# Performance work log

Hardware: AMD Instinct MI355X
Metric: run time of the kernel (lower is better)

Reference implementation:

```python
import jax, jax.numpy as jnp
import numpy as np

IN_F = 4096
OUT_F = 4096

def setup_inputs() -> dict:
    key = jax.random.key(0)
    k1, k2 = jax.random.split(key)
    x = jax.random.normal(k1, (4, 2048, IN_F), dtype=jnp.float32)
    W = jax.random.normal(k2, (OUT_F, IN_F), dtype=jnp.float32) * (1.0 / np.sqrt(IN_F))
    return {"x": x, "W": W}

def reference(x, W):
    # per-tensor scale = mean |W|, clamped
    scale = jnp.maximum(jnp.mean(jnp.abs(W)), 1e-8)
    # pentanet: 5-level quantization {-2,-1,0,1,2}
    w_quant = jnp.clip(jnp.round(W / scale), -2.0, 2.0)
    # STE: forward uses quantized weights, gradient flows to W
    w_ste = jax.lax.stop_gradient(w_quant * scale - W) + W
    # F.linear: x @ w_ste.T -> [b, s, out]
    return jnp.einsum('bsi,oi->bso', x, w_ste)
```

## Files before the change

kernel.cpp:

```cpp
#include <hip/hip_runtime.h>
#include <cstdint>
#include <cstddef>

#define IN_F 4096
#define OUT_F 4096

typedef __attribute__((ext_vector_type(8))) short bf16x8;
typedef __attribute__((ext_vector_type(4))) float f32x4;

__device__ __forceinline__ ushort f32_bf16_rne(float f) {
    uint32_t u = __builtin_bit_cast(uint32_t, f);
    uint32_t r = (u + 0x7FFFu + ((u >> 16) & 1u)) >> 16;
    return (ushort)r;
}

__device__ __forceinline__ void gload_lds16(const void* g, void* l) {
    __builtin_amdgcn_global_load_lds(
        (const __attribute__((address_space(1))) uint32_t*)g,
        (__attribute__((address_space(3))) uint32_t*)l,
        16, 0, 0);
}

__device__ __forceinline__ void fenced_barrier() {
    asm volatile("" ::: "memory");
    __builtin_amdgcn_sched_barrier(0);
    __builtin_amdgcn_s_barrier();
    __builtin_amdgcn_sched_barrier(0);
    asm volatile("" ::: "memory");
}

__global__ void reduce_abs1(const float* __restrict__ W, float* __restrict__ part) {
    __shared__ float sm[256];
    const int b = blockIdx.x, t = threadIdx.x;
    const float* p = W + (size_t)b * 4096;
    float s = 0.f;
#pragma unroll
    for (int j = 0; j < 16; ++j) s += fabsf(p[t + 256 * j]);
    sm[t] = s;
    __syncthreads();
    for (int w = 128; w > 0; w >>= 1) {
        if (t < w) sm[t] += sm[t + w];
        __syncthreads();
    }
    if (t == 0) part[b] = sm[0];
}

__global__ void reduce_abs2(const float* __restrict__ part, float* __restrict__ scale) {
    __shared__ float sm[256];
    const int t = threadIdx.x;
    float s = 0.f;
#pragma unroll
    for (int j = 0; j < 16; ++j) s += part[t + 256 * j];
    sm[t] = s;
    __syncthreads();
    for (int w = 128; w > 0; w >>= 1) {
        if (t < w) sm[t] += sm[t + w];
        __syncthreads();
    }
    if (t == 0) {
        float m = sm[0] / 16777216.0f;
        *scale = fmaxf(m, 1e-8f);
    }
}

__global__ void quantize_w(const float* __restrict__ W, ushort* __restrict__ wq,
                           const float* __restrict__ scale_p) {
    const int i = blockIdx.x * 256 + threadIdx.x;
    const float s = *scale_p;
    float4 v = ((const float4*)W)[i];
    float q0 = fminf(fmaxf(rintf(v.x / s), -2.f), 2.f);
    float q1 = fminf(fmaxf(rintf(v.y / s), -2.f), 2.f);
    float q2 = fminf(fmaxf(rintf(v.z / s), -2.f), 2.f);
    float q3 = fminf(fmaxf(rintf(v.w / s), -2.f), 2.f);
    ushort4 o;
    o.x = f32_bf16_rne(q0); o.y = f32_bf16_rne(q1);
    o.z = f32_bf16_rne(q2); o.w = f32_bf16_rne(q3);
    ((ushort4*)wq)[i] = o;
}

__global__ void cast_x(const float* __restrict__ X, ushort* __restrict__ xh) {
    const int i = blockIdx.x * 256 + threadIdx.x;
    float4 v = ((const float4*)X)[i];
    ushort4 o;
    o.x = f32_bf16_rne(v.x); o.y = f32_bf16_rne(v.y);
    o.z = f32_bf16_rne(v.z); o.w = f32_bf16_rne(v.w);
    ((ushort4*)xh)[i] = o;
}

#define BK 64
#define HT_BYTES 16384
#define BUF_BYTES 65536

__global__ __launch_bounds__(512, 2) void qgemm256(
        const ushort* __restrict__ Ab, const ushort* __restrict__ Bq,
        float* __restrict__ C, const float* __restrict__ scale_p,
        int M, int N, int K) {
    extern __shared__ __align__(16) char smem[];

    const int t = threadIdx.x;
    const int lane = t & 63;
    const int w = t >> 6;
    const int wr = w >> 2;
    const int wc = w & 3;
    const int bh = wc >> 1;

    const int nwg = gridDim.x;
    int wg = blockIdx.x;
    if ((nwg & 7) == 0) wg = (wg & 7) * (nwg >> 3) + (wg >> 3);
    const int MT = M >> 8;
    const int m0 = (wg % MT) << 8;
    const int n0 = (wg / MT) << 8;

    const int NT = K / BK;
    const int NS = NT * 4;

    int pre[2];
#pragma unroll
    for (int ks = 0; ks < 2; ++ks)
        pre[ks] = (lane & 15) * 128 +
                  (((ks * 64) + ((lane >> 4) * 16)) ^ ((lane & 7) << 4));

    auto do_stage = [&](int s) {
        if (s >= NS) return;
        const int kt = s >> 2, h = s & 3;
        const int k0 = kt * BK;
        char* region;
        const ushort* gsrc;
        if (h < 2) {
            region = smem + (kt & 1) * BUF_BYTES + 32768 + h * HT_BYTES;
            gsrc = Bq + (size_t)(n0 + h * 128) * K + k0;
        } else {
            region = smem + (kt & 1) * BUF_BYTES + (h - 2) * HT_BYTES;
            gsrc = Ab + (size_t)(m0 + (h - 2) * 128) * K + k0;
        }
#pragma unroll
        for (int j = 0; j < 2; ++j) {
            int e = j * 4096 + t * 8;
            int r = e >> 6, c8 = (e >> 3) & 7;
            int srcc = (c8 ^ (r & 7)) * 8;
            gload_lds16(gsrc + (size_t)r * K + srcc, region + e * 2);
        }
    };

    f32x4 acc[8][4];
#pragma unroll
    for (int m = 0; m < 8; ++m)
#pragma unroll
        for (int n = 0; n < 4; ++n) acc[m][n] = (f32x4){0.f, 0.f, 0.f, 0.f};

    do_stage(0); do_stage(1); do_stage(2); do_stage(3);
    asm volatile("s_waitcnt vmcnt(4)");
    do_stage(4); do_stage(5); do_stage(6);
    asm volatile("s_waitcnt vmcnt(6)");
    fenced_barrier();

    for (int kt = 0; kt < NT; ++kt) {
        const char* aB = smem + (kt & 1) * BUF_BYTES + wr * HT_BYTES;
        const char* bB = smem + (kt & 1) * BUF_BYTES + 32768 + bh * HT_BYTES +
                         (wc & 1) * 8192;
        const int sbase = 7 + kt * 4;

        bf16x8 bfr[4][2], a0[4][2], a1[4][2];

#pragma unroll
        for (int n = 0; n < 4; ++n)
#pragma unroll
            for (int ks = 0; ks < 2; ++ks)
                bfr[n][ks] = *(const bf16x8*)(bB + n * 2048 + pre[ks]);
#pragma unroll
        for (int m = 0; m < 4; ++m)
#pragma unroll
            for (int ks = 0; ks < 2; ++ks)
                a0[m][ks] = *(const bf16x8*)(aB + m * 2048 + pre[ks]);
        do_stage(sbase + 0);
        fenced_barrier();
        __builtin_amdgcn_s_setprio(1);
#pragma unroll
        for (int m = 0; m < 4; ++m)
#pragma unroll
            for (int n = 0; n < 2; ++n)
#pragma unroll
                for (int ks = 0; ks < 2; ++ks)
                    acc[m][n] = __builtin_amdgcn_mfma_f32_16x16x32_bf16(
                        a0[m][ks], bfr[n][ks], acc[m][n], 0, 0, 0);
        __builtin_amdgcn_s_setprio(0);
        fenced_barrier();

#pragma unroll
        for (int m = 0; m < 4; ++m)
#pragma unroll
            for (int ks = 0; ks < 2; ++ks)
                a1[m][ks] = *(const bf16x8*)(aB + (m + 4) * 2048 + pre[ks]);
        do_stage(sbase + 1);
        fenced_barrier();
        __builtin_amdgcn_s_setprio(1);
#pragma unroll
        for (int m = 0; m < 4; ++m)
#pragma unroll
            for (int n = 2; n < 4; ++n)
#pragma unroll
                for (int ks = 0; ks < 2; ++ks)
                    acc[m][n] = __builtin_amdgcn_mfma_f32_16x16x32_bf16(
                        a0[m][ks], bfr[n][ks], acc[m][n], 0, 0, 0);
        __builtin_amdgcn_s_setprio(0);
        fenced_barrier();

        do_stage(sbase + 2);
        fenced_barrier();
        __builtin_amdgcn_s_setprio(1);
#pragma unroll
        for (int m = 0; m < 4; ++m)
#pragma unroll
            for (int n = 0; n < 2; ++n)
#pragma unroll
                for (int ks = 0; ks < 2; ++ks)
                    acc[m + 4][n] = __builtin_amdgcn_mfma_f32_16x16x32_bf16(
                        a1[m][ks], bfr[n][ks], acc[m + 4][n], 0, 0, 0);
        __builtin_amdgcn_s_setprio(0);
        fenced_barrier();

        do_stage(sbase + 3);
        fenced_barrier();
        __builtin_amdgcn_s_setprio(1);
#pragma unroll
        for (int m = 0; m < 4; ++m)
#pragma unroll
            for (int n = 2; n < 4; ++n)
#pragma unroll
                for (int ks = 0; ks < 2; ++ks)
                    acc[m + 4][n] = __builtin_amdgcn_mfma_f32_16x16x32_bf16(
                        a1[m][ks], bfr[n][ks], acc[m + 4][n], 0, 0, 0);
        __builtin_amdgcn_s_setprio(0);
        if (kt < NT - 2) {
            asm volatile("s_waitcnt vmcnt(6)");
        } else if (kt == NT - 2) {
            asm volatile("s_waitcnt vmcnt(0)");
        }
        fenced_barrier();
    }

    const float s = *scale_p;
#pragma unroll
    for (int m = 0; m < 8; ++m)
#pragma unroll
        for (int n = 0; n < 4; ++n) {
            const int col = n0 + wc * 64 + n * 16 + (lane & 15);
            const int rbase = m0 + wr * 128 + m * 16 + ((lane >> 4) << 2);
#pragma unroll
            for (int j = 0; j < 4; ++j)
                C[(size_t)(rbase + j) * N + col] = s * acc[m][n][j];
        }
}

template <bool ABF16>
__global__ __launch_bounds__(256) void qgemm(const void* __restrict__ Aptr,
                                             const ushort* __restrict__ Bq,
                                             float* __restrict__ C,
                                             const float* __restrict__ scale_p,
                                             int M, int N, int K) {
    __shared__ __align__(16) ushort sA[128 * 64];
    __shared__ __align__(16) ushort sB[128 * 64];

    const int t = threadIdx.x;
    const int lane = t & 63;
    const int w = t >> 6;
    const int wr = w >> 1, wc = w & 1;

    const int nwg = gridDim.x;
    int wg = blockIdx.x;
    if ((nwg & 7) == 0) wg = (wg & 7) * (nwg >> 3) + (wg >> 3);
    const int MT = M >> 7;
    const int mt = wg % MT;
    const int nt = wg / MT;
    const int m0 = mt * 128, n0 = nt * 128;

    const ushort* Ab = (const ushort*)Aptr;
    const float* Af = (const float*)Aptr;

    f32x4 zero = {0.f, 0.f, 0.f, 0.f};
    f32x4 acc[4][4];
#pragma unroll
    for (int m = 0; m < 4; ++m)
#pragma unroll
        for (int n = 0; n < 4; ++n) acc[m][n] = zero;

    for (int k0 = 0; k0 < K; k0 += 64) {
#pragma unroll
        for (int i = 0; i < 4; ++i) {
            int e = i * 2048 + t * 8;
            int r = e >> 6, c8 = (e >> 3) & 7;
            int srcc = (c8 ^ (r & 7)) * 8;
            gload_lds16(Bq + (size_t)(n0 + r) * K + (k0 + srcc), &sB[e]);
        }
        if constexpr (ABF16) {
#pragma unroll
            for (int i = 0; i < 4; ++i) {
                int e = i * 2048 + t * 8;
                int r = e >> 6, c8 = (e >> 3) & 7;
                int srcc = (c8 ^ (r & 7)) * 8;
                gload_lds16(Ab + (size_t)(m0 + r) * K + (k0 + srcc), &sA[e]);
            }
        } else {
#pragma unroll
            for (int i = 0; i < 4; ++i) {
                int e = i * 2048 + t * 8;
                int r = e >> 6, c = e & 63;
                const float* src = Af + (size_t)(m0 + r) * K + (k0 + c);
                float4 v0 = *(const float4*)src;
                float4 v1 = *(const float4*)(src + 4);
                bf16x8 pk;
                pk[0] = (short)f32_bf16_rne(v0.x); pk[1] = (short)f32_bf16_rne(v0.y);
                pk[2] = (short)f32_bf16_rne(v0.z); pk[3] = (short)f32_bf16_rne(v0.w);
                pk[4] = (short)f32_bf16_rne(v1.x); pk[5] = (short)f32_bf16_rne(v1.y);
                pk[6] = (short)f32_bf16_rne(v1.z); pk[7] = (short)f32_bf16_rne(v1.w);
                int byte = (r * 128 + c * 2) ^ ((r & 7) << 4);
                *(bf16x8*)((char*)sA + byte) = pk;
            }
        }
        __syncthreads();

#pragma unroll
        for (int ks = 0; ks < 2; ++ks) {
            const int kk = ks * 32 + ((lane >> 4) << 3);
            bf16x8 afr[4], bfr[4];
#pragma unroll
            for (int m = 0; m < 4; ++m) {
                int r = wr * 64 + m * 16 + (lane & 15);
                int byte = (r * 128 + kk * 2) ^ ((r & 7) << 4);
                afr[m] = *(const bf16x8*)((const char*)sA + byte);
            }
#pragma unroll
            for (int n = 0; n < 4; ++n) {
                int r = wc * 64 + n * 16 + (lane & 15);
                int byte = (r * 128 + kk * 2) ^ ((r & 7) << 4);
                bfr[n] = *(const bf16x8*)((const char*)sB + byte);
            }
#pragma unroll
            for (int m = 0; m < 4; ++m)
#pragma unroll
                for (int n = 0; n < 4; ++n)
                    acc[m][n] = __builtin_amdgcn_mfma_f32_16x16x32_bf16(
                        afr[m], bfr[n], acc[m][n], 0, 0, 0);
        }
        __syncthreads();
    }

    const float s = *scale_p;
#pragma unroll
    for (int m = 0; m < 4; ++m)
#pragma unroll
        for (int n = 0; n < 4; ++n) {
            const int col = n0 + wc * 64 + n * 16 + (lane & 15);
            const int rbase = m0 + wr * 64 + m * 16 + ((lane >> 4) << 2);
#pragma unroll
            for (int j = 0; j < 4; ++j)
                C[(size_t)(rbase + j) * N + col] = s * acc[m][n][j];
        }
}

__global__ void naive_qgemm(const float* __restrict__ X, const float* __restrict__ W,
                            float* __restrict__ out, const float* __restrict__ scale_p,
                            int M) {
    const int col = blockIdx.x * 256 + threadIdx.x;
    const int row = blockIdx.y;
    const float s = *scale_p;
    const float inv = 1.0f / s;
    const float* xr = X + (size_t)row * IN_F;
    const float* wrow = W + (size_t)col * IN_F;
    float acc = 0.f;
    for (int k = 0; k < IN_F; ++k) {
        float q = fminf(fmaxf(rintf(wrow[k] * inv), -2.f), 2.f);
        acc += xr[k] * q;
    }
    out[(size_t)row * OUT_F + col] = acc * s;
}

extern "C" void kernel_launch(void* const* d_in, const int* in_sizes, int n_in,
                              void* d_out, int out_size, void* d_ws, size_t ws_size,
                              hipStream_t stream) {
    const float* x = (const float*)d_in[0];
    const float* W = (const float*)d_in[1];
    float* out = (float*)d_out;
    const int M = in_sizes[0] / IN_F;
    const int K = IN_F, N = OUT_F;

    char* ws = (char*)d_ws;
    const size_t OFF_PART = 512;
    const size_t OFF_WQ = OFF_PART + 4096 * sizeof(float);
    const size_t WQ_BYTES = (size_t)N * K * sizeof(ushort);
    const size_t OFF_XH = OFF_WQ + WQ_BYTES;
    const size_t XH_BYTES = (size_t)M * K * sizeof(ushort);
    float* scale = (float*)(ws + 0);
    float* part = (float*)(ws + OFF_PART);
    ushort* wq = (ushort*)(ws + OFF_WQ);
    ushort* xh = (ushort*)(ws + OFF_XH);

    if (ws_size < OFF_WQ) return;

    reduce_abs1<<<4096, 256, 0, stream>>>(W, part);
    reduce_abs2<<<1, 256, 0, stream>>>(part, scale);

    if (ws_size >= OFF_XH + XH_BYTES && (M % 256) == 0 && (N % 256) == 0) {
        quantize_w<<<(N * K / 4) / 256, 256, 0, stream>>>(W, wq, scale);
        cast_x<<<(M * K / 4) / 256, 256, 0, stream>>>(x, xh);
        (void)hipFuncSetAttribute((const void*)qgemm256,
                                  hipFuncAttributeMaxDynamicSharedMemorySize,
                                  131072);
        qgemm256<<<(M / 256) * (N / 256), 512, 131072, stream>>>(
            xh, wq, out, scale, M, N, K);
    } else if (ws_size >= OFF_XH + XH_BYTES) {
        quantize_w<<<(N * K / 4) / 256, 256, 0, stream>>>(W, wq, scale);
        cast_x<<<(M * K / 4) / 256, 256, 0, stream>>>(x, xh);
        qgemm<true><<<(M / 128) * (N / 128), 256, 0, stream>>>(xh, wq, out, scale, M, N, K);
    } else if (ws_size >= OFF_WQ + WQ_BYTES) {
        quantize_w<<<(N * K / 4) / 256, 256, 0, stream>>>(W, wq, scale);
        qgemm<false><<<(M / 128) * (N / 128), 256, 0, stream>>>(x, wq, out, scale, M, N, K);
    } else {
        naive_qgemm<<<dim3(N / 256, M), 256, 0, stream>>>(x, W, out, scale, M);
    }
}
```

Before: 338.4 us.

## Reorder GEMM stage schedule, split B fragment loads, and lighten barriers

Swaps the staging order so the A halves are issued before the B halves within each k-tile. The B-fragment LDS reads are split into two halves, and the MFMA quadrants are reordered so the second half of B is read later, overlapping it with compute. The sched_barrier-fenced barrier is replaced by a plain inline-asm s_barrier with a memory clobber, and a redundant prologue waitcnt is dropped. The intent is to shorten LDS-read stalls and give the compiler more scheduling freedom, at the risk of subtle hazards in buffer reuse ordering.

```diff
diff --git a/kernel.cpp b/kernel.cpp
--- a/kernel.cpp
+++ b/kernel.cpp
@@ -21,12 +21,8 @@
         16, 0, 0);
 }
 
-__device__ __forceinline__ void fenced_barrier() {
-    asm volatile("" ::: "memory");
-    __builtin_amdgcn_sched_barrier(0);
-    __builtin_amdgcn_s_barrier();
-    __builtin_amdgcn_sched_barrier(0);
-    asm volatile("" ::: "memory");
+__device__ __forceinline__ void bar() {
+    asm volatile("s_barrier" ::: "memory");
 }
 
 __global__ void reduce_abs1(const float* __restrict__ W, float* __restrict__ part) {
@@ -124,14 +120,15 @@
         if (s >= NS) return;
         const int kt = s >> 2, h = s & 3;
         const int k0 = kt * BK;
+        char* bufbase = smem + (kt & 1) * BUF_BYTES;
         char* region;
         const ushort* gsrc;
         if (h < 2) {
-            region = smem + (kt & 1) * BUF_BYTES + 32768 + h * HT_BYTES;
-            gsrc = Bq + (size_t)(n0 + h * 128) * K + k0;
+            region = bufbase + h * HT_BYTES;
+            gsrc = Ab + (size_t)(m0 + h * 128) * K + k0;
         } else {
-            region = smem + (kt & 1) * BUF_BYTES + (h - 2) * HT_BYTES;
-            gsrc = Ab + (size_t)(m0 + (h - 2) * 128) * K + k0;
+            region = bufbase + 32768 + (h - 2) * HT_BYTES;
+            gsrc = Bq + (size_t)(n0 + (h - 2) * 128) * K + k0;
         }
 #pragma unroll
         for (int j = 0; j < 2; ++j) {
@@ -149,10 +146,9 @@
         for (int n = 0; n < 4; ++n) acc[m][n] = (f32x4){0.f, 0.f, 0.f, 0.f};
 
     do_stage(0); do_stage(1); do_stage(2); do_stage(3);
-    asm volatile("s_waitcnt vmcnt(4)");
     do_stage(4); do_stage(5); do_stage(6);
-    asm volatile("s_waitcnt vmcnt(6)");
-    fenced_barrier();
+    asm volatile("s_waitcnt vmcnt(6)" ::: "memory");
+    bar();
 
     for (int kt = 0; kt < NT; ++kt) {
         const char* aB = smem + (kt & 1) * BUF_BYTES + wr * HT_BYTES;
@@ -163,7 +159,7 @@
         bf16x8 bfr[4][2], a0[4][2], a1[4][2];
 
 #pragma unroll
-        for (int n = 0; n < 4; ++n)
+        for (int n = 0; n < 2; ++n)
 #pragma unroll
             for (int ks = 0; ks < 2; ++ks)
                 bfr[n][ks] = *(const bf16x8*)(bB + n * 2048 + pre[ks]);
@@ -173,7 +169,7 @@
             for (int ks = 0; ks < 2; ++ks)
                 a0[m][ks] = *(const bf16x8*)(aB + m * 2048 + pre[ks]);
         do_stage(sbase + 0);
-        fenced_barrier();
+        bar();
         __builtin_amdgcn_s_setprio(1);
 #pragma unroll
         for (int m = 0; m < 4; ++m)
@@ -184,7 +180,7 @@
                     acc[m][n] = __builtin_amdgcn_mfma_f32_16x16x32_bf16(
                         a0[m][ks], bfr[n][ks], acc[m][n], 0, 0, 0);
         __builtin_amdgcn_s_setprio(0);
-        fenced_barrier();
+        bar();
 
 #pragma unroll
         for (int m = 0; m < 4; ++m)
@@ -192,7 +188,26 @@
             for (int ks = 0; ks < 2; ++ks)
                 a1[m][ks] = *(const bf16x8*)(aB + (m + 4) * 2048 + pre[ks]);
         do_stage(sbase + 1);
-        fenced_barrier();
+        bar();
+        __builtin_amdgcn_s_setprio(1);
+#pragma unroll
+        for (int m = 0; m < 4; ++m)
+#pragma unroll
+            for (int n = 0; n < 2; ++n)
+#pragma unroll
+                for (int ks = 0; ks < 2; ++ks)
+                    acc[m + 4][n] = __builtin_amdgcn_mfma_f32_16x16x32_bf16(
+                        a1[m][ks], bfr[n][ks], acc[m + 4][n], 0, 0, 0);
+        __builtin_amdgcn_s_setprio(0);
+        bar();
+
+#pragma unroll
+        for (int n = 2; n < 4; ++n)
+#pragma unroll
+            for (int ks = 0; ks < 2; ++ks)
+                bfr[n][ks] = *(const bf16x8*)(bB + n * 2048 + pre[ks]);
+        do_stage(sbase + 2);
+        bar();
         __builtin_amdgcn_s_setprio(1);
 #pragma unroll
         for (int m = 0; m < 4; ++m)
@@ -203,24 +218,10 @@
                     acc[m][n] = __builtin_amdgcn_mfma_f32_16x16x32_bf16(
                         a0[m][ks], bfr[n][ks], acc[m][n], 0, 0, 0);
         __builtin_amdgcn_s_setprio(0);
-        fenced_barrier();
-
-        do_stage(sbase + 2);
-        fenced_barrier();
-        __builtin_amdgcn_s_setprio(1);
-#pragma unroll
-        for (int m = 0; m < 4; ++m)
-#pragma unroll
-            for (int n = 0; n < 2; ++n)
-#pragma unroll
-                for (int ks = 0; ks < 2; ++ks)
-                    acc[m + 4][n] = __builtin_amdgcn_mfma_f32_16x16x32_bf16(
-                        a1[m][ks], bfr[n][ks], acc[m + 4][n], 0, 0, 0);
-        __builtin_amdgcn_s_setprio(0);
-        fenced_barrier();
+        bar();
 
         do_stage(sbase + 3);
-        fenced_barrier();
+        bar();
         __builtin_amdgcn_s_setprio(1);
 #pragma unroll
         for (int m = 0; m < 4; ++m)
@@ -232,11 +233,11 @@
                         a1[m][ks], bfr[n][ks], acc[m + 4][n], 0, 0, 0);
         __builtin_amdgcn_s_setprio(0);
         if (kt < NT - 2) {
-            asm volatile("s_waitcnt vmcnt(6)");
+            asm volatile("s_waitcnt vmcnt(6)" ::: "memory");
         } else if (kt == NT - 2) {
-            asm volatile("s_waitcnt vmcnt(0)");
-        }
-        fenced_barrier();
+            asm volatile("s_waitcnt vmcnt(0)" ::: "memory");
+        }
+        bar();
     }
 
     const float s = *scale_p;
```

Measured after the change: 337.1 us. No clear change (-0.4%).
